# Kernel tuning notes

Hardware: AMD Instinct MI355X
Metric: run time of the kernel (lower is better)

The kernel has to match this reference:

```python
import jax, jax.numpy as jnp
import numpy as np

D_MODEL = 1024
N_HEADS = 16
HEAD_DIM = D_MODEL // N_HEADS
FFN = 4096
NUM_REL = 64
BATCH = 4
SEQ = 1024
EPS = 1e-6


def _layernorm(x, g, b):
    mu = jnp.mean(x, axis=-1, keepdims=True)
    var = jnp.mean(jnp.square(x - mu), axis=-1, keepdims=True)
    return (x - mu) * jax.lax.rsqrt(var + EPS) * g + b


def setup_inputs() -> dict:
    key = jax.random.key(0)
    ks = jax.random.split(key, 16)
    s_d = 1.0 / np.sqrt(D_MODEL)
    s_f = 1.0 / np.sqrt(FFN)
    inp = {
        "x": jax.random.normal(ks[0], (BATCH, SEQ, D_MODEL), jnp.float32),
        "relative_ids": jax.random.randint(ks[1], (SEQ, SEQ), 0, NUM_REL),
        # attention projections (row-major: y = x @ W + b)
        "Wq": jax.random.normal(ks[2], (D_MODEL, D_MODEL), jnp.float32) * s_d,
        "bq": jnp.zeros((D_MODEL,), jnp.float32),
        "Wk": jax.random.normal(ks[3], (D_MODEL, D_MODEL), jnp.float32) * s_d,
        "bk": jnp.zeros((D_MODEL,), jnp.float32),
        "Wv": jax.random.normal(ks[4], (D_MODEL, D_MODEL), jnp.float32) * s_d,
        "bv": jnp.zeros((D_MODEL,), jnp.float32),
        "Wo": jax.random.normal(ks[5], (D_MODEL, D_MODEL), jnp.float32) * s_d,
        "bo": jnp.zeros((D_MODEL,), jnp.float32),
        # relative position tables: Ek for keys (rel-e), Eb per-head bias (rel-b)
        "Ek": jax.random.normal(ks[6], (NUM_REL, HEAD_DIM), jnp.float32) * (1.0 / np.sqrt(HEAD_DIM)),
        "Eb": jax.random.normal(ks[7], (NUM_REL, N_HEADS), jnp.float32) * 0.02,
        # layernorms
        "g1": jnp.ones((D_MODEL,), jnp.float32),
        "b1": jnp.zeros((D_MODEL,), jnp.float32),
        "g2": jnp.ones((D_MODEL,), jnp.float32),
        "b2": jnp.zeros((D_MODEL,), jnp.float32),
        # FFN
        "W1": jax.random.normal(ks[8], (D_MODEL, FFN), jnp.float32) * s_d,
        "bf1": jnp.zeros((FFN,), jnp.float32),
        "W2": jax.random.normal(ks[9], (FFN, D_MODEL), jnp.float32) * s_f,
        "bf2": jnp.zeros((D_MODEL,), jnp.float32),
    }
    return inp


def _forward(x, relative_ids, Wq, bq, Wk, bk, Wv, bv, Wo, bo, Ek, Eb,
             g1, b1, g2, b2, W1, bf1, W2, bf2):
    B, S, D = x.shape
    # projections -> [B, H, S, Dh]
    def split_heads(t):
        return t.reshape(B, S, N_HEADS, HEAD_DIM).transpose(0, 2, 1, 3)
    q = split_heads(x @ Wq + bq)
    k = split_heads(x @ Wk + bk)
    v = split_heads(x @ Wv + bv)

    scores = jnp.einsum('bhqd,bhkd->bhqk', q, k)
    # rel-e: relative key embeddings interact with queries
    Erel = Ek[relative_ids]                      # [S, S, Dh]
    scores = scores + jnp.einsum('bhqd,qkd->bhqk', q, Erel)
    # rel-b: per-head relative bias
    scores = scores + Eb[relative_ids].transpose(2, 0, 1)[None]  # [1,H,S,S]
    scores = scores / jnp.sqrt(jnp.asarray(HEAD_DIM, x.dtype))

    attn = jax.nn.softmax(scores, axis=-1)
    ctx = jnp.einsum('bhqk,bhkd->bhqd', attn, v)
    ctx = ctx.transpose(0, 2, 1, 3).reshape(B, S, D)
    a_out = ctx @ Wo + bo

    # dropout is identity at eval
    ff_in = _layernorm(x + a_out, g1, b1)
    ff = jax.nn.relu(ff_in @ W1 + bf1) @ W2 + bf2
    return _layernorm(ff_in + ff, g2, b2)


def reference(x, relative_ids, Wq, bq, Wk, bk, Wv, bv, Wo, bo, Ek, Eb,
              g1, b1, g2, b2, W1, bf1, W2, bf2):
    return _forward(x, relative_ids, Wq, bq, Wk, bk, Wv, bv, Wo, bo, Ek, Eb,
                    g1, b1, g2, b2, W1, bf1, W2, bf2)
```

## Files before the change

kernel.cpp:

```cpp
#include <hip/hip_runtime.h>


typedef short bf16x8 __attribute__((ext_vector_type(8)));
typedef float f32x4 __attribute__((ext_vector_type(4)));

#define DEVI static __device__ __forceinline__

constexpr int SEQ = 1024, DMODEL = 1024, NH = 16, HDIM = 64, FFDIM = 4096, NREL = 64, NBATCH = 4;
constexpr int ROWS = NBATCH * SEQ;
#define QSC 0.18033688011112042f

DEVI unsigned short f2b(float f) {
  union { float f; unsigned u; } v; v.f = f;
  unsigned r = v.u + 0x7FFFu + ((v.u >> 16) & 1u);
  return (unsigned short)(r >> 16);
}

DEVI float b2f(unsigned short u) {
  union { unsigned v; float f; } x; x.v = (unsigned)u << 16; return x.f;
}

#if __has_builtin(__builtin_amdgcn_cvt_pk_bf16_f32)
DEVI unsigned pack2(float a, float b) {
  auto r = __builtin_amdgcn_cvt_pk_bf16_f32(a, b);
  return __builtin_bit_cast(unsigned, r);
}
#else
DEVI unsigned pack2(float a, float b) {
  return (unsigned)f2b(a) | ((unsigned)f2b(b) << 16);
}
#endif

DEVI float fexp2(float x) {
#if __has_builtin(__builtin_amdgcn_exp2f)
  return __builtin_amdgcn_exp2f(x);
#else
  return exp2f(x);
#endif
}

DEVI float4 ld4h(const unsigned short* p) {
  uint2 u = *(const uint2*)p;
  union { unsigned v; float f; } a, b, c, d;
  a.v = u.x << 16; b.v = u.x & 0xffff0000u; c.v = u.y << 16; d.v = u.y & 0xffff0000u;
  return make_float4(a.f, b.f, c.f, d.f);
}

DEVI void gload16(const unsigned short* g, unsigned short* l) {
  __builtin_amdgcn_global_load_lds((const __attribute__((address_space(1))) void*)g,
                                   (__attribute__((address_space(3))) void*)l, 16, 0, 0);
}

template <int BM, int BN>
DEVI void g256_core(const unsigned short* __restrict__ A, int lda,
                    const unsigned short* __restrict__ Bt, int ldb, int K,
                    unsigned short* S, f32x4* acc) {
  constexpr int MT = BM / 32, NT = BN / 64;
  constexpr int LOADS = BM / 64 + BN / 64;
  constexpr int SBUF = (BM + BN) * 64;
  const int tid = threadIdx.x, wave = tid >> 6, lane = tid & 63;
  const int wm = wave & 1, wn = wave >> 1;
  const int lr = lane & 15, kq = lane >> 4;
  const int srow = lane >> 3, schunk = (lane & 7) ^ (srow & 7);
  const int sw = lr & 7;

  const f32x4 zero = {0.f, 0.f, 0.f, 0.f};
#pragma unroll
  for (int i = 0; i < MT * NT; ++i) acc[i] = zero;

  const unsigned short* ga = A + (size_t)(wave * (BM / 8) + srow) * lda + schunk * 8;
  const unsigned short* gb = Bt + (size_t)(wave * (BN / 8) + srow) * ldb + schunk * 8;
  unsigned short* dA = S + wave * (BM / 8) * 64;
  unsigned short* dB = S + BM * 64 + wave * (BN / 8) * 64;

#define STG(buf, k0)                                                         \
  do {                                                                       \
    _Pragma("unroll") for (int j = 0; j < BM / 64; ++j)                      \
        gload16(ga + (size_t)(j * 8) * lda + (k0), dA + (buf)*SBUF + j * 8 * 64); \
    _Pragma("unroll") for (int j = 0; j < BN / 64; ++j)                      \
        gload16(gb + (size_t)(j * 8) * ldb + (k0), dB + (buf)*SBUF + j * 8 * 64); \
  } while (0)

  STG(0, 0);
  STG(1, 64);

  const unsigned short* pa = S + (wm * (BM / 2) + lr) * 64;
  const unsigned short* pb = S + BM * 64 + (wn * (BN / 4) + lr) * 64;
  const int nt = K >> 6;

  for (int t = 0; t < nt; ++t) {
    const int buf = t & 1;
    if (t < nt - 1) {
      if constexpr (LOADS == 8) {
        asm volatile("s_waitcnt vmcnt(8)" ::: "memory");
      } else {
        asm volatile("s_waitcnt vmcnt(6)" ::: "memory");
      }
    } else {
      asm volatile("s_waitcnt vmcnt(0)" ::: "memory");
    }
    __builtin_amdgcn_s_barrier();
    asm volatile("" ::: "memory");
    const unsigned short* qa = pa + buf * SBUF;
    const unsigned short* qb = pb + buf * SBUF;
#pragma unroll
    for (int ks = 0; ks < 2; ++ks) {
      const int rc = ((ks * 4 + kq) ^ sw) * 8;
      bf16x8 af[MT], bv[NT];
#pragma unroll
      for (int mi = 0; mi < MT; ++mi) af[mi] = *(const bf16x8*)(qa + mi * 16 * 64 + rc);
#pragma unroll
      for (int ni = 0; ni < NT; ++ni) bv[ni] = *(const bf16x8*)(qb + ni * 16 * 64 + rc);
#pragma unroll
      for (int mi = 0; mi < MT; ++mi)
#pragma unroll
        for (int ni = 0; ni < NT; ++ni)
          acc[mi * NT + ni] =
              __builtin_amdgcn_mfma_f32_16x16x32_bf16(af[mi], bv[ni], acc[mi * NT + ni], 0, 0, 0);
    }
    asm volatile("" ::: "memory");
    __builtin_amdgcn_s_barrier();
    asm volatile("" ::: "memory");
    if (t + 2 < nt) STG(buf, (t + 2) * 64);
  }
#undef STG
}

template <int BN2, bool RELU, bool SPLITK>
__global__ __launch_bounds__(512, 2) void k_g256(const unsigned short* __restrict__ A, int lda,
                                                 const unsigned short* __restrict__ Bt, int ldb,
                                                 int K, int N, const float* __restrict__ bias,
                                                 unsigned short* __restrict__ outh,
                                                 size_t ostride) {
  constexpr int BM = 256, MT = 8, NT = BN2 / 64;
  __shared__ __align__(16) unsigned short S[2 * (BM + BN2) * 64];
  f32x4 acc[MT * NT];
  const int m0 = blockIdx.y * BM, n0 = blockIdx.x * BN2;
  const int kc = SPLITK ? blockIdx.z : 0;
  g256_core<BM, BN2>(A + (size_t)m0 * lda + (size_t)kc * K, lda,
                     Bt + (size_t)n0 * ldb + (size_t)kc * K, ldb, K, S, acc);
  if (SPLITK) outh += (size_t)kc * ostride;
  const int tid = threadIdx.x, wave = tid >> 6, lane = tid & 63;
  const int wm = wave & 1, wn = wave >> 1, lr = lane & 15, kq = lane >> 4;
#pragma unroll
  for (int mi = 0; mi < MT; ++mi) {
    const int row0 = m0 + wm * 128 + mi * 16 + kq * 4;
#pragma unroll
    for (int ni = 0; ni < NT; ++ni) {
      const int col = n0 + wn * (BN2 / 4) + ni * 16 + lr;
      const float bc = (!SPLITK || kc == 0) ? bias[col] : 0.f;
      f32x4 v = acc[mi * NT + ni];
#pragma unroll
      for (int r = 0; r < 4; ++r) {
        float y = v[r] + bc;
        if (RELU) y = fmaxf(y, 0.f);
        outh[(size_t)(row0 + r) * N + col] = f2b(y);
      }
    }
  }
}

__global__ __launch_bounds__(512, 2) void k_proj256(
    const unsigned short* __restrict__ A, const unsigned short* __restrict__ WqT,
    const unsigned short* __restrict__ WkT, const unsigned short* __restrict__ WvT,
    const float* __restrict__ bq, const float* __restrict__ bk, const float* __restrict__ bv,
    unsigned short* __restrict__ oq, unsigned short* __restrict__ ok,
    unsigned short* __restrict__ ov) {
  __shared__ __align__(16) unsigned short S[2 * 512 * 64];
  f32x4 acc[32];
  const int which = blockIdx.z;
  const unsigned short* Bt = which == 0 ? WqT : which == 1 ? WkT : WvT;
  const float* bias = which == 0 ? bq : which == 1 ? bk : bv;
  unsigned short* out = which == 0 ? oq : which == 1 ? ok : ov;
  const float scl = which == 0 ? QSC : 1.0f;
  const int m0 = blockIdx.y * 256, n0 = blockIdx.x * 256;
  g256_core<256, 256>(A + (size_t)m0 * DMODEL, DMODEL, Bt + (size_t)n0 * DMODEL, DMODEL, DMODEL,
                      S, acc);
  const int tid = threadIdx.x, wave = tid >> 6, lane = tid & 63;
  const int wm = wave & 1, wn = wave >> 1, lr = lane & 15, kq = lane >> 4;
#pragma unroll
  for (int mi = 0; mi < 8; ++mi) {
    const int row0 = m0 + wm * 128 + mi * 16 + kq * 4;
    const int b = row0 >> 10, s0 = row0 & 1023;
#pragma unroll
    for (int ni = 0; ni < 4; ++ni) {
      const int col = n0 + wn * 64 + ni * 16 + lr;
      const int h = col >> 6, d = col & 63;
      const float bc = bias[col];
      f32x4 v = acc[mi * 4 + ni];
#pragma unroll
      for (int r = 0; r < 4; ++r) v[r] = (v[r] + bc) * scl;
      if (which != 2) {
#pragma unroll
        for (int r = 0; r < 4; ++r)
          out[((size_t)((b * NH + h) * SEQ) + s0 + r) * HDIM + d] = f2b(v[r]);
      } else {
        uint2 p = make_uint2(pack2(v[0], v[1]), pack2(v[2], v[3]));
        *(uint2*)&out[((size_t)((b * NH + h) * HDIM) + d) * SEQ + s0] = p;
      }
    }
  }
}

__global__ __launch_bounds__(256, 4) void k_flash(const unsigned short* __restrict__ q,
                                                  const unsigned short* __restrict__ kk,
                                                  const unsigned short* __restrict__ vT,
                                                  const unsigned short* __restrict__ Ekb,
                                                  const float* __restrict__ Eb,
                                                  const unsigned char* __restrict__ rel8,
                                                  unsigned short* __restrict__ ctx) {
  __shared__ __align__(16) unsigned short sK[128 * 64];
  __shared__ __align__(16) unsigned short sV[64 * 128];
  __shared__ __align__(16) unsigned short sqEB16[64 * 62];
  __shared__ float sRow[4][16];

  const int tid = threadIdx.x, wave = tid >> 6, lane = tid & 63;
  const int lr = lane & 15, kq = lane >> 4;

  const int L = blockIdx.y * 16 + blockIdx.x;
  const int xcd = L & 7, idx = L >> 3;
  const int z = xcd * 8 + (idx >> 4), qt = idx & 15;
  const int b = z >> 4, h = z & 15;
  const size_t zo = (size_t)z * SEQ * HDIM;
  const size_t vo = (size_t)z * HDIM * SEQ;

  const int srow8 = lane >> 3, sl8 = lane & 7;
  const int sw8 = sl8 ^ (srow8 & 7);
  const int dl = lane >> 4, sl16 = lane & 15;
  const int swl = lr & 7;
  const f32x4 zero = {0.f, 0.f, 0.f, 0.f};

  unsigned short* sQv = sV;
#pragma unroll
  for (int j = 0; j < 2; ++j) {
    const int row = wave * 16 + j * 8 + srow8;
    gload16(q + zo + (size_t)(qt * 64 + row) * 64 + sw8 * 8, sQv + (wave * 16 + j * 8) * 64);
    gload16(Ekb + (size_t)row * 64 + sw8 * 8, sK + (wave * 16 + j * 8) * 64);
  }
  __syncthreads();

  bf16x8 bq_[2];
#pragma unroll
  for (int ks = 0; ks < 2; ++ks)
    bq_[ks] = *(const bf16x8*)&sQv[(wave * 16 + lr) * 64 + (((ks * 4 + kq) ^ swl) << 3)];

  {
    f32x4 accE[4];
#pragma unroll
    for (int nf = 0; nf < 4; ++nf) accE[nf] = zero;
#pragma unroll
    for (int ks = 0; ks < 2; ++ks) {
#pragma unroll
      for (int nf = 0; nf < 4; ++nf) {
        bf16x8 ek = *(const bf16x8*)&sK[(nf * 16 + lr) * 64 + (((ks * 4 + kq) ^ swl) << 3)];
        accE[nf] = __builtin_amdgcn_mfma_f32_16x16x32_bf16(bq_[ks], ek, accE[nf], 0, 0, 0);
      }
    }
#pragma unroll
    for (int nf = 0; nf < 4; ++nf) {
      const int rid = nf * 16 + lr;
      const float eb = Eb[rid * NH + h] * QSC;
      const int base = rid * 62 + wave * 16 + kq * 4;
      *(unsigned*)&sqEB16[base] = pack2(accE[nf][0] + eb, accE[nf][1] + eb);
      *(unsigned*)&sqEB16[base + 2] = pack2(accE[nf][2] + eb, accE[nf][3] + eb);
    }
  }

  float l_run = 0.f;
  f32x4 accO[4];
#pragma unroll
  for (int nd = 0; nd < 4; ++nd) accO[nd] = zero;
  const int qrow_g = qt * 64 + wave * 16 + lr;
  const unsigned char* relrow8 = rel8 + (size_t)qrow_g * SEQ;
  const int qcol = wave * 16 + lr;
  unsigned short* sPw = sK + wave * 2048;

  for (int kt = 0; kt < 8; ++kt) {
    __syncthreads();
#pragma unroll
    for (int j = 0; j < 4; ++j) {
      const int row = wave * 32 + j * 8 + srow8;
      gload16(kk + zo + (size_t)(kt * 128 + row) * 64 + sw8 * 8, sK + (wave * 32 + j * 8) * 64);
    }
#pragma unroll
    for (int j = 0; j < 4; ++j) {
      const int row = wave * 16 + j * 4 + dl;
      const int ch = sl16 ^ (row & 15);
      gload16(vT + vo + (size_t)row * SEQ + kt * 128 + ch * 8, sV + (wave * 16 + j * 4) * 128);
    }
    unsigned ru[8];
#pragma unroll
    for (int mi = 0; mi < 8; ++mi)
      ru[mi] = *(const unsigned*)&relrow8[kt * 128 + mi * 16 + kq * 4];
    __syncthreads();

    f32x4 accS[8];
#pragma unroll
    for (int mi = 0; mi < 8; ++mi) accS[mi] = zero;
#pragma unroll
    for (int ks = 0; ks < 2; ++ks) {
#pragma unroll
      for (int mi = 0; mi < 8; ++mi) {
        bf16x8 a = *(const bf16x8*)&sK[(mi * 16 + lr) * 64 + (((ks * 4 + kq) ^ swl) << 3)];
        accS[mi] = __builtin_amdgcn_mfma_f32_16x16x32_bf16(a, bq_[ks], accS[mi], 0, 0, 0);
      }
    }
#pragma unroll
    for (int mi = 0; mi < 8; ++mi) {
      const float p0 = fexp2(accS[mi][0] + b2f(sqEB16[(int)(ru[mi] & 255u) * 62 + qcol]));
      const float p1 = fexp2(accS[mi][1] + b2f(sqEB16[(int)((ru[mi] >> 8) & 255u) * 62 + qcol]));
      const float p2 = fexp2(accS[mi][2] + b2f(sqEB16[(int)((ru[mi] >> 16) & 255u) * 62 + qcol]));
      const float p3 = fexp2(accS[mi][3] + b2f(sqEB16[(int)(ru[mi] >> 24) * 62 + qcol]));
      accS[mi][0] = p0; accS[mi][1] = p1; accS[mi][2] = p2; accS[mi][3] = p3;
      l_run += (p0 + p1) + (p2 + p3);
    }
    __syncthreads();

#pragma unroll
    for (int mi = 0; mi < 8; ++mi) {
      const int c = 2 * mi + (kq >> 1);
      *(uint2*)&sPw[lr * 128 + ((c ^ lr) << 3) + ((kq & 1) << 2)] =
          make_uint2(pack2(accS[mi][0], accS[mi][1]), pack2(accS[mi][2], accS[mi][3]));
    }
#pragma unroll
    for (int kst = 0; kst < 4; ++kst) {
      const int cc = ((kq + 4 * kst) ^ lr) << 3;
      bf16x8 a = *(const bf16x8*)&sPw[lr * 128 + cc];
#pragma unroll
      for (int nd = 0; nd < 4; ++nd) {
        bf16x8 bv = *(const bf16x8*)&sV[(nd * 16 + lr) * 128 + cc];
        accO[nd] = __builtin_amdgcn_mfma_f32_16x16x32_bf16(a, bv, accO[nd], 0, 0, 0);
      }
    }
  }

  l_run += __shfl_xor(l_run, 16);
  l_run += __shfl_xor(l_run, 32);
  if (kq == 0) sRow[wave][lr] = l_run;
  const float4 lv = *(const float4*)&sRow[wave][kq * 4];
  const float inv[4] = {1.f / lv.x, 1.f / lv.y, 1.f / lv.z, 1.f / lv.w};
  const size_t rbase = (size_t)(b * SEQ + qt * 64 + wave * 16 + kq * 4);
#pragma unroll
  for (int nd = 0; nd < 4; ++nd) {
    const int col = h * HDIM + nd * 16 + lr;
#pragma unroll
    for (int r = 0; r < 4; ++r)
      ctx[(rbase + r) * DMODEL + col] = f2b(accO[nd][r] * inv[r]);
  }
}

template <bool WB>
__global__ __launch_bounds__(256) void k_addln3(const unsigned short* __restrict__ a,
                                                const unsigned short* __restrict__ p0,
                                                const unsigned short* __restrict__ p1,
                                                const float* __restrict__ g,
                                                const float* __restrict__ beta,
                                                float* __restrict__ outf,
                                                unsigned short* __restrict__ outh) {
  const int row = blockIdx.x, t = threadIdx.x;
  const size_t base = (size_t)row * DMODEL + t * 4;
  float4 va = ld4h(&a[base]);
  float4 v0 = ld4h(&p0[base]);
  float4 v1 = ld4h(&p1[base]);
  const float x0 = va.x + v0.x + v1.x, x1 = va.y + v0.y + v1.y;
  const float x2 = va.z + v0.z + v1.z, x3 = va.w + v0.w + v1.w;
  __shared__ float red[4];
  float s = x0 + x1 + x2 + x3;
#pragma unroll
  for (int o = 32; o; o >>= 1) s += __shfl_xor(s, o);
  if ((t & 63) == 0) red[t >> 6] = s;
  __syncthreads();
  const float mu = (red[0] + red[1] + red[2] + red[3]) * (1.0f / DMODEL);
  __syncthreads();
  const float d0 = x0 - mu, d1 = x1 - mu, d2 = x2 - mu, d3 = x3 - mu;
  float qv = d0 * d0 + d1 * d1 + d2 * d2 + d3 * d3;
#pragma unroll
  for (int o = 32; o; o >>= 1) qv += __shfl_xor(qv, o);
  if ((t & 63) == 0) red[t >> 6] = qv;
  __syncthreads();
  const float var = (red[0] + red[1] + red[2] + red[3]) * (1.0f / DMODEL);
  const float sc = rsqrtf(var + 1e-6f);
  float4 vg = *(const float4*)&g[t * 4];
  float4 ve = *(const float4*)&beta[t * 4];
  float4 y;
  y.x = d0 * sc * vg.x + ve.x;
  y.y = d1 * sc * vg.y + ve.y;
  y.z = d2 * sc * vg.z + ve.z;
  y.w = d3 * sc * vg.w + ve.w;
  if (WB) {
    uint2 p = make_uint2(pack2(y.x, y.y), pack2(y.z, y.w));
    *(uint2*)&outh[base] = p;
  } else {
    *(float4*)&outf[base] = y;
  }
}

__global__ __launch_bounds__(256) void k_tcast12(
    const float* __restrict__ Wq, const float* __restrict__ Wk, const float* __restrict__ Wv,
    const float* __restrict__ Wo, const float* __restrict__ W1, const float* __restrict__ W2,
    unsigned short* __restrict__ oq, unsigned short* __restrict__ ok,
    unsigned short* __restrict__ ov, unsigned short* __restrict__ oo,
    unsigned short* __restrict__ o1, unsigned short* __restrict__ o2) {
  const int z = blockIdx.z;
  const float* in;
  unsigned short* out;
  int ldi, ldo;
  if (z < 4) {
    in = z == 0 ? Wq : z == 1 ? Wk : z == 2 ? Wv : Wo;
    out = z == 0 ? oq : z == 1 ? ok : z == 2 ? ov : oo;
    ldi = 1024; ldo = 1024;
  } else if (z < 8) {
    const int s = z - 4;
    in = W1 + (size_t)s * 1024; ldi = 4096;
    out = o1 + (size_t)s * 1024 * 1024; ldo = 1024;
  } else {
    const int s = z - 8;
    in = W2 + (size_t)s * 1024 * 1024; ldi = 1024;
    out = o2 + (size_t)s * 1024; ldo = 4096;
  }
  __shared__ float tile[32][33];
  const int tx = threadIdx.x & 31, ty = threadIdx.x >> 5;
  const int r0 = blockIdx.y * 32, c0 = blockIdx.x * 32;
#pragma unroll
  for (int i = 0; i < 4; ++i)
    tile[ty + i * 8][tx] = in[(size_t)(r0 + ty + i * 8) * ldi + c0 + tx];
  __syncthreads();
#pragma unroll
  for (int i = 0; i < 4; ++i)
    out[(size_t)(c0 + ty + i * 8) * ldo + r0 + tx] = f2b(tile[tx][ty + i * 8]);
}

__global__ __launch_bounds__(256) void k_cast2(const float* __restrict__ a,
                                               unsigned short* __restrict__ oa, int n4a,
                                               const float* __restrict__ bsrc,
                                               unsigned short* __restrict__ ob, int n4b,
                                               const int* __restrict__ rel,
                                               unsigned char* __restrict__ r8, int n4c) {
  const int i = blockIdx.x * 256 + threadIdx.x;
  if (i < n4a) {
    float4 v = *(const float4*)&a[(size_t)i * 4];
    uint2 p = make_uint2(pack2(v.x, v.y), pack2(v.z, v.w));
    *(uint2*)&oa[(size_t)i * 4] = p;
  } else {
    const int j = i - n4a;
    if (j < n4b) {
      float4 v = *(const float4*)&bsrc[(size_t)j * 4];
      uint2 p = make_uint2(pack2(v.x, v.y), pack2(v.z, v.w));
      *(uint2*)&ob[(size_t)j * 4] = p;
    } else {
      const int k2 = j - n4b;
      if (k2 < n4c) {
        int4 v = *(const int4*)&rel[(size_t)k2 * 4];
        unsigned pk = (unsigned)(v.x & 255) | ((unsigned)(v.y & 255) << 8) |
                      ((unsigned)(v.z & 255) << 16) | ((unsigned)(v.w & 255) << 24);
        *(unsigned*)&r8[(size_t)k2 * 4] = pk;
      }
    }
  }
}


extern "C" void kernel_launch(void* const* d_in, const int* in_sizes, int n_in, void* d_out,
                              int out_size, void* d_ws, size_t ws_size, hipStream_t stream) {
  const float* x = (const float*)d_in[0];
  const int* rel = (const int*)d_in[1];
  const float* Wq = (const float*)d_in[2];
  const float* bq = (const float*)d_in[3];
  const float* Wk = (const float*)d_in[4];
  const float* bk = (const float*)d_in[5];
  const float* Wv = (const float*)d_in[6];
  const float* bv = (const float*)d_in[7];
  const float* Wo = (const float*)d_in[8];
  const float* bo = (const float*)d_in[9];
  const float* Ek = (const float*)d_in[10];
  const float* Eb = (const float*)d_in[11];
  const float* g1 = (const float*)d_in[12];
  const float* b1 = (const float*)d_in[13];
  const float* g2 = (const float*)d_in[14];
  const float* b2 = (const float*)d_in[15];
  const float* W1 = (const float*)d_in[16];
  const float* bf1 = (const float*)d_in[17];
  const float* W2 = (const float*)d_in[18];
  const float* bf2 = (const float*)d_in[19];
  float* out = (float*)d_out;

  char* ws = (char*)d_ws;
  const size_t MB = 1ull << 20;
  unsigned short* Wqt = (unsigned short*)(ws + 0 * MB);
  unsigned short* Wkt = (unsigned short*)(ws + 2 * MB);
  unsigned short* Wvt = (unsigned short*)(ws + 4 * MB);
  unsigned short* Wot = (unsigned short*)(ws + 6 * MB);
  unsigned short* W1t = (unsigned short*)(ws + 8 * MB);
  unsigned short* W2t = (unsigned short*)(ws + 16 * MB);
  unsigned short* xb = (unsigned short*)(ws + 24 * MB);
  unsigned short* Ekb = (unsigned short*)(ws + 32 * MB);
  unsigned short* qbuf = (unsigned short*)(ws + 33 * MB);
  unsigned short* kbuf = (unsigned short*)(ws + 41 * MB);
  unsigned short* vTb = (unsigned short*)(ws + 49 * MB);
  unsigned short* ctx = (unsigned short*)(ws + 57 * MB);
  unsigned short* Pb = (unsigned short*)(ws + 65 * MB);
  unsigned char* rel8 = (unsigned char*)(ws + 65 * MB);
  unsigned short* ff_in_b = (unsigned short*)(ws + 81 * MB);
  unsigned short* hidden = (unsigned short*)(ws + 89 * MB);
  const size_t OST = (size_t)ROWS * DMODEL;

  k_tcast12<<<dim3(32, 32, 12), 256, 0, stream>>>(Wq, Wk, Wv, Wo, W1, W2, Wqt, Wkt, Wvt, Wot,
                                                  W1t, W2t);
  k_cast2<<<5124, 256, 0, stream>>>(x, xb, ROWS * DMODEL / 4, Ek, Ekb, NREL * HDIM / 4, rel, rel8,
                                    SEQ * SEQ / 4);

  k_proj256<<<dim3(4, 16, 3), 512, 0, stream>>>(xb, Wqt, Wkt, Wvt, bq, bk, bv, qbuf, kbuf, vTb);

  k_flash<<<dim3(16, 64), 256, 0, stream>>>(qbuf, kbuf, vTb, Ekb, Eb, rel8, ctx);

  k_g256<128, false, true><<<dim3(8, 16, 2), 512, 0, stream>>>(ctx, DMODEL, Wot, DMODEL,
                                                               DMODEL / 2, DMODEL, bo, Pb, OST);
  k_addln3<true><<<ROWS, 256, 0, stream>>>(xb, Pb, Pb + OST, g1, b1, nullptr, ff_in_b);

  k_g256<256, true, false><<<dim3(FFDIM / 256, ROWS / 256), 512, 0, stream>>>(
      ff_in_b, DMODEL, W1t, DMODEL, DMODEL, FFDIM, bf1, hidden, 0);
  k_g256<128, false, true><<<dim3(8, 16, 2), 512, 0, stream>>>(hidden, FFDIM, W2t, FFDIM,
                                                               FFDIM / 2, DMODEL, bf2, Pb, OST);
  k_addln3<false><<<ROWS, 256, 0, stream>>>(ff_in_b, Pb, Pb + OST, g2, b2, out, nullptr);
}
```

Measured before the change: 342.1 us.

## Add XCD-aware block remap and triple-buffered LDS for split-K GEMMs

```diff
diff --git a/kernel.cpp b/kernel.cpp
--- a/kernel.cpp
+++ b/kernel.cpp
@@ -51,7 +51,12 @@
                                    (__attribute__((address_space(3))) void*)l, 16, 0, 0);
 }
 
-template <int BM, int BN>
+DEVI int xcd_work(int nwg) {
+  const int L = (blockIdx.z * gridDim.y + blockIdx.y) * gridDim.x + blockIdx.x;
+  return (L & 7) * (nwg >> 3) + (L >> 3);
+}
+
+template <int BM, int BN, int NBUF>
 DEVI void g256_core(const unsigned short* __restrict__ A, int lda,
                     const unsigned short* __restrict__ Bt, int ldb, int K,
                     unsigned short* S, f32x4* acc) {
@@ -88,8 +93,8 @@
   const unsigned short* pb = S + BM * 64 + (wn * (BN / 4) + lr) * 64;
   const int nt = K >> 6;
 
+  int buf = 0, nxt = 2 % NBUF;
   for (int t = 0; t < nt; ++t) {
-    const int buf = t & 1;
     if (t < nt - 1) {
       if constexpr (LOADS == 8) {
         asm volatile("s_waitcnt vmcnt(8)" ::: "memory");
@@ -119,26 +124,36 @@
               __builtin_amdgcn_mfma_f32_16x16x32_bf16(af[mi], bv[ni], acc[mi * NT + ni], 0, 0, 0);
     }
     asm volatile("" ::: "memory");
-    __builtin_amdgcn_s_barrier();
-    asm volatile("" ::: "memory");
-    if (t + 2 < nt) STG(buf, (t + 2) * 64);
+    if constexpr (NBUF == 2) {
+      __builtin_amdgcn_s_barrier();
+      asm volatile("" ::: "memory");
+      if (t + 2 < nt) STG(buf, (t + 2) * 64);
+    } else {
+      if (t + 2 < nt) STG(nxt, (t + 2) * 64);
+    }
+    buf = (buf == NBUF - 1) ? 0 : buf + 1;
+    nxt = (nxt == NBUF - 1) ? 0 : nxt + 1;
   }
 #undef STG
 }
 
-template <int BN2, bool RELU, bool SPLITK>
+template <int BN2, bool RELU, bool SPLITK, int NBUF = 2>
 __global__ __launch_bounds__(512, 2) void k_g256(const unsigned short* __restrict__ A, int lda,
                                                  const unsigned short* __restrict__ Bt, int ldb,
                                                  int K, int N, const float* __restrict__ bias,
                                                  unsigned short* __restrict__ outh,
                                                  size_t ostride) {
   constexpr int BM = 256, MT = 8, NT = BN2 / 64;
-  __shared__ __align__(16) unsigned short S[2 * (BM + BN2) * 64];
+  __shared__ __align__(16) unsigned short S[NBUF * (BM + BN2) * 64];
   f32x4 acc[MT * NT];
-  const int m0 = blockIdx.y * BM, n0 = blockIdx.x * BN2;
-  const int kc = SPLITK ? blockIdx.z : 0;
-  g256_core<BM, BN2>(A + (size_t)m0 * lda + (size_t)kc * K, lda,
-                     Bt + (size_t)n0 * ldb + (size_t)kc * K, ldb, K, S, acc);
+  const int gx = gridDim.x, gy = gridDim.y;
+  const int W = xcd_work(gx * gy * gridDim.z);
+  const int bx = W % gx, rem = W / gx;
+  const int by = rem % gy, bz = rem / gy;
+  const int m0 = by * BM, n0 = bx * BN2;
+  const int kc = SPLITK ? bz : 0;
+  g256_core<BM, BN2, NBUF>(A + (size_t)m0 * lda + (size_t)kc * K, lda,
+                           Bt + (size_t)n0 * ldb + (size_t)kc * K, ldb, K, S, acc);
   if (SPLITK) outh += (size_t)kc * ostride;
   const int tid = threadIdx.x, wave = tid >> 6, lane = tid & 63;
   const int wm = wave & 1, wn = wave >> 1, lr = lane & 15, kq = lane >> 4;
@@ -168,14 +183,17 @@
     unsigned short* __restrict__ ov) {
   __shared__ __align__(16) unsigned short S[2 * 512 * 64];
   f32x4 acc[32];
-  const int which = blockIdx.z;
+  const int gx = gridDim.x, gy = gridDim.y;
+  const int W = xcd_work(gx * gy * gridDim.z);
+  const int bx = W % gx, rem = W / gx;
+  const int by = rem % gy, which = rem / gy;
   const unsigned short* Bt = which == 0 ? WqT : which == 1 ? WkT : WvT;
   const float* bias = which == 0 ? bq : which == 1 ? bk : bv;
   unsigned short* out = which == 0 ? oq : which == 1 ? ok : ov;
   const float scl = which == 0 ? QSC : 1.0f;
-  const int m0 = blockIdx.y * 256, n0 = blockIdx.x * 256;
-  g256_core<256, 256>(A + (size_t)m0 * DMODEL, DMODEL, Bt + (size_t)n0 * DMODEL, DMODEL, DMODEL,
-                      S, acc);
+  const int m0 = by * 256, n0 = bx * 256;
+  g256_core<256, 256, 2>(A + (size_t)m0 * DMODEL, DMODEL, Bt + (size_t)n0 * DMODEL, DMODEL,
+                         DMODEL, S, acc);
   const int tid = threadIdx.x, wave = tid >> 6, lane = tid & 63;
   const int wm = wave & 1, wn = wave >> 1, lr = lane & 15, kq = lane >> 4;
 #pragma unroll
@@ -513,13 +531,13 @@
 
   k_flash<<<dim3(16, 64), 256, 0, stream>>>(qbuf, kbuf, vTb, Ekb, Eb, rel8, ctx);
 
-  k_g256<128, false, true><<<dim3(8, 16, 2), 512, 0, stream>>>(ctx, DMODEL, Wot, DMODEL,
-                                                               DMODEL / 2, DMODEL, bo, Pb, OST);
+  k_g256<128, false, true, 3><<<dim3(8, 16, 2), 512, 0, stream>>>(ctx, DMODEL, Wot, DMODEL,
+                                                                  DMODEL / 2, DMODEL, bo, Pb, OST);
   k_addln3<true><<<ROWS, 256, 0, stream>>>(xb, Pb, Pb + OST, g1, b1, nullptr, ff_in_b);
 
-  k_g256<256, true, false><<<dim3(FFDIM / 256, ROWS / 256), 512, 0, stream>>>(
+  k_g256<256, true, false, 2><<<dim3(FFDIM / 256, ROWS / 256), 512, 0, stream>>>(
       ff_in_b, DMODEL, W1t, DMODEL, DMODEL, FFDIM, bf1, hidden, 0);
-  k_g256<128, false, true><<<dim3(8, 16, 2), 512, 0, stream>>>(hidden, FFDIM, W2t, FFDIM,
-                                                               FFDIM / 2, DMODEL, bf2, Pb, OST);
+  k_g256<128, false, true, 3><<<dim3(8, 16, 2), 512, 0, stream>>>(hidden, FFDIM, W2t, FFDIM,
+                                                                  FFDIM / 2, DMODEL, bf2, Pb, OST);
   k_addln3<false><<<ROWS, 256, 0, stream>>>(ff_in_b, Pb, Pb + OST, g2, b2, out, nullptr);
 }
```

Measured after the change: 335.4 us. 2.0% less time.
